# Kernel optimization log

Measured on AMD Instinct MI355X. Metric: run time of the kernel, lower is better.

The kernel has to match this reference:

```python
import jax, jax.numpy as jnp
import numpy as np

N = 100000
E = 1600000
NFEAT, NHID, NCLASS = 500, 128, 40


def setup_inputs() -> dict:
    key = jax.random.key(0)
    ks = jax.random.split(key, 12)
    x = jax.random.normal(ks[0], (N, NFEAT), dtype=jnp.float32)
    row = jax.random.randint(ks[1], (E,), 0, N, dtype=jnp.int32)
    col = jax.random.randint(ks[2], (E,), 0, N, dtype=jnp.int32)
    # precomputed normalized adjacency values (D^-1/2 A D^-1/2 style)
    edge_weight = jax.random.uniform(ks[3], (E,), dtype=jnp.float32) / 16.0
    def lin(k, fi, fo):
        s = 1.0 / np.sqrt(fi)
        return jax.random.uniform(k, (fi, fo), dtype=jnp.float32, minval=-s, maxval=s)
    return {
        "x": x, "row": row, "col": col, "edge_weight": edge_weight,
        "W1": lin(ks[4], NFEAT, NHID), "b1": jnp.zeros((NHID,), jnp.float32),
        "W2": lin(ks[5], NHID, NHID), "b2": jnp.zeros((NHID,), jnp.float32),
        "W3": lin(ks[6], NHID, NHID), "b3": jnp.zeros((NHID,), jnp.float32),
        "W4": lin(ks[7], NHID, NCLASS), "b4": jnp.zeros((NCLASS,), jnp.float32),
    }


def gcn_layer(h, row, col, edge_weight, W, b):
    # support = h @ W ; out = spmm(adj, support) + b  (Kipf GraphConvolution)
    support = h @ W                                   # [N, Fout]
    msgs = edge_weight[:, None] * support[col]        # [E, Fout] gather on source nodes
    agg = jax.ops.segment_sum(msgs, row, num_segments=N)  # scatter-add to dest nodes
    return agg + b


def reference(x, row, col, edge_weight, W1, b1, W2, b2, W3, b3, W4, b4):
    # dropout is identity in eval mode (training=False)
    h = jax.nn.relu(gcn_layer(x, row, col, edge_weight, W1, b1))
    h = jax.nn.relu(gcn_layer(h, row, col, edge_weight, W2, b2))
    h = jax.nn.relu(gcn_layer(h, row, col, edge_weight, W3, b3))
    h = gcn_layer(h, row, col, edge_weight, W4, b4)
    return jax.nn.log_softmax(h, axis=1)
```

## Files before the change

kernel.cpp:

```cpp
#include <hip/hip_runtime.h>
#include <cstdint>
#include <cstddef>

#define NFEAT 500
#define NHID  128
#define NCLASS 40

typedef __attribute__((ext_vector_type(8))) short bf16x8;
typedef __attribute__((ext_vector_type(4))) float f32x4;

__device__ __forceinline__ unsigned short f2bf(float f) {
    union { float f; unsigned u; } v; v.f = f;
    unsigned u = v.u;
    unsigned r = u + 0x7FFF + ((u >> 16) & 1);
    return (unsigned short)(r >> 16);
}
__device__ __forceinline__ float bf2f(unsigned short h) {
    union { unsigned u; float f; } v; v.u = ((unsigned)h) << 16; return v.f;
}


__global__ void k_hist(const int* __restrict__ row, int E, int* __restrict__ counts) {
    int i = blockIdx.x * 256 + threadIdx.x;
    if (i < E) atomicAdd(&counts[row[i]], 1);
}

__global__ void k_block_sum(const int* __restrict__ counts, int n, int* __restrict__ partials) {
    __shared__ int tmp[256];
    int i = blockIdx.x * 256 + threadIdx.x;
    tmp[threadIdx.x] = (i < n) ? counts[i] : 0;
    __syncthreads();
    for (int o = 128; o > 0; o >>= 1) {
        if (threadIdx.x < o) tmp[threadIdx.x] += tmp[threadIdx.x + o];
        __syncthreads();
    }
    if (threadIdx.x == 0) partials[blockIdx.x] = tmp[0];
}

__global__ void k_scan_partials(int* __restrict__ partials, int nb) {
    __shared__ int tmp[512];
    int t = threadIdx.x;
    int v = (t < nb) ? partials[t] : 0;
    tmp[t] = v;
    __syncthreads();
    for (int o = 1; o < 512; o <<= 1) {
        int add = (t >= o) ? tmp[t - o] : 0;
        __syncthreads();
        tmp[t] += add;
        __syncthreads();
    }
    if (t < nb) partials[t] = tmp[t] - v;
}

__global__ void k_scan_counts(int* __restrict__ counts, const int* __restrict__ partials,
                              int* __restrict__ row_ptr, int n) {
    __shared__ int tmp[256];
    int t = threadIdx.x;
    int i = blockIdx.x * 256 + t;
    int v = (i < n) ? counts[i] : 0;
    tmp[t] = v;
    __syncthreads();
    for (int o = 1; o < 256; o <<= 1) {
        int add = (t >= o) ? tmp[t - o] : 0;
        __syncthreads();
        tmp[t] += add;
        __syncthreads();
    }
    int incl = tmp[t];
    int base = partials[blockIdx.x];
    if (i < n) {
        row_ptr[i] = base + incl - v;
        counts[i] = 0;
    }
    if (i == n - 1) row_ptr[n] = base + incl;
}

__global__ void k_scatter(const int* __restrict__ row, const int* __restrict__ col,
                          const float* __restrict__ w, int E,
                          const int* __restrict__ row_ptr, int* __restrict__ cursor,
                          uint2* __restrict__ csr_cw) {
    int i = blockIdx.x * 256 + threadIdx.x;
    if (i < E) {
        int r = row[i];
        int p = row_ptr[r] + atomicAdd(&cursor[r], 1);
        csr_cw[p] = make_uint2((unsigned)col[i], __float_as_uint(w[i]));
    }
}


__global__ void k_prep_w(const float* __restrict__ W, unsigned short* __restrict__ Wt,
                         int K, int Norig, int Nt, int Kpad) {
    int idx = blockIdx.x * 256 + threadIdx.x;
    if (idx >= Nt * Kpad) return;
    int n = idx / Kpad, k = idx % Kpad;
    unsigned short v = 0;
    if (k < K && n < Norig) v = f2bf(W[(size_t)k * Norig + n]);
    Wt[idx] = v;
}


template<bool AFP32, int BN, int CN, int CPITCH>
__global__ __launch_bounds__(256) void k_gemm_mfma(const void* __restrict__ Ain,
                                                   const unsigned short* __restrict__ Wt,
                                                   unsigned short* __restrict__ C,
                                                   int M, int K, int Kpad) {
    constexpr int P = 40;
    constexpr int WGN = (BN == 128) ? 2 : 1;
    constexpr int WGM = 4 / WGN;
    constexpr int TM = 128 / (WGM * 16);
    constexpr int TN = BN / (WGN * 16);
    __shared__ unsigned short As[128][P];
    __shared__ unsigned short Ws[BN][P];

    const int t = threadIdx.x;
    const int lane = t & 63;
    const int w = t >> 6;
    const int wm = w / WGN, wn = w % WGN;
    const int mbase = blockIdx.x * 128;
    const int l15 = lane & 15, quad = lane >> 4;

    const float* Af = (const float*)Ain;
    const unsigned short* Ab = (const unsigned short*)Ain;

    f32x4 acc[TM][TN];
#pragma unroll
    for (int mi = 0; mi < TM; mi++)
#pragma unroll
        for (int ni = 0; ni < TN; ni++)
            acc[mi][ni] = (f32x4){0.f, 0.f, 0.f, 0.f};

    for (int k0 = 0; k0 < Kpad; k0 += 32) {
        if (AFP32) {
#pragma unroll
            for (int p = 0; p < 4; p++) {
                int idx = p * 256 + t;
                int m = idx >> 3, k4 = idx & 7;
                int gm = mbase + m, gk = k0 + k4 * 4;
                float4 v = make_float4(0.f, 0.f, 0.f, 0.f);
                if (gm < M) {
                    if (gk + 3 < K) {
                        v = *(const float4*)(Af + (size_t)gm * K + gk);
                    } else {
                        float tmp[4] = {0.f, 0.f, 0.f, 0.f};
                        for (int j = 0; j < 4; j++)
                            if (gk + j < K) tmp[j] = Af[(size_t)gm * K + gk + j];
                        v = make_float4(tmp[0], tmp[1], tmp[2], tmp[3]);
                    }
                }
                unsigned long long pk = (unsigned long long)f2bf(v.x)
                                      | ((unsigned long long)f2bf(v.y) << 16)
                                      | ((unsigned long long)f2bf(v.z) << 32)
                                      | ((unsigned long long)f2bf(v.w) << 48);
                *(unsigned long long*)&As[m][k4 * 4] = pk;
            }
        } else {
#pragma unroll
            for (int p = 0; p < 2; p++) {
                int idx = p * 256 + t;
                int m = idx >> 2, ch = idx & 3;
                int gm = mbase + m, gk = k0 + ch * 8;
                uint4 v = make_uint4(0u, 0u, 0u, 0u);
                if (gm < M) v = *(const uint4*)(Ab + (size_t)gm * K + gk);
                *(uint4*)&As[m][ch * 8] = v;
            }
        }
        for (int idx = t; idx < BN * 4; idx += 256) {
            int n = idx >> 2, ch = idx & 3;
            uint4 v = *(const uint4*)(Wt + (size_t)n * Kpad + k0 + ch * 8);
            *(uint4*)&Ws[n][ch * 8] = v;
        }
        __syncthreads();

        bf16x8 afr[TM], bfr[TN];
#pragma unroll
        for (int mi = 0; mi < TM; mi++)
            afr[mi] = *(const bf16x8*)&As[wm * (TM * 16) + mi * 16 + l15][quad * 8];
#pragma unroll
        for (int ni = 0; ni < TN; ni++)
            bfr[ni] = *(const bf16x8*)&Ws[wn * (TN * 16) + ni * 16 + l15][quad * 8];
#pragma unroll
        for (int mi = 0; mi < TM; mi++)
#pragma unroll
            for (int ni = 0; ni < TN; ni++)
                acc[mi][ni] = __builtin_amdgcn_mfma_f32_16x16x32_bf16(afr[mi], bfr[ni], acc[mi][ni], 0, 0, 0);
        __syncthreads();
    }

#pragma unroll
    for (int mi = 0; mi < TM; mi++) {
#pragma unroll
        for (int r = 0; r < 4; r++) {
            int gm = mbase + wm * (TM * 16) + mi * 16 + quad * 4 + r;
            if (gm < M) {
#pragma unroll
                for (int ni = 0; ni < TN; ni++) {
                    int gn = wn * (TN * 16) + ni * 16 + l15;
                    if (gn < CN) C[(size_t)gm * CPITCH + gn] = f2bf(acc[mi][ni][r]);
                }
            }
        }
    }
}


__global__ __launch_bounds__(256) void k_spmm128(const unsigned short* __restrict__ S,
                                                 const int* __restrict__ rp,
                                                 const uint2* __restrict__ cw,
                                                 const float* __restrict__ bias,
                                                 unsigned short* __restrict__ out,
                                                 int n, int do_relu) {
    int wid  = threadIdx.x >> 6;
    int lane = threadIdx.x & 63;
    int node = blockIdx.x * 4 + wid;
    if (node >= n) return;
    int s = rp[node], e = rp[node + 1];
    float a0x = 0.f, a0y = 0.f, a1x = 0.f, a1y = 0.f;
    float a2x = 0.f, a2y = 0.f, a3x = 0.f, a3y = 0.f;
    int i = s;
    for (; i + 4 <= e; i += 4) {
        uint2 e0 = cw[i], e1 = cw[i + 1], e2 = cw[i + 2], e3 = cw[i + 3];
        unsigned v0 = ((const unsigned*)(S + (size_t)e0.x * NHID))[lane];
        unsigned v1 = ((const unsigned*)(S + (size_t)e1.x * NHID))[lane];
        unsigned v2 = ((const unsigned*)(S + (size_t)e2.x * NHID))[lane];
        unsigned v3 = ((const unsigned*)(S + (size_t)e3.x * NHID))[lane];
        float w0 = __uint_as_float(e0.y), w1 = __uint_as_float(e1.y);
        float w2 = __uint_as_float(e2.y), w3 = __uint_as_float(e3.y);
        a0x = fmaf(w0, bf2f((unsigned short)v0), a0x); a0y = fmaf(w0, bf2f((unsigned short)(v0 >> 16)), a0y);
        a1x = fmaf(w1, bf2f((unsigned short)v1), a1x); a1y = fmaf(w1, bf2f((unsigned short)(v1 >> 16)), a1y);
        a2x = fmaf(w2, bf2f((unsigned short)v2), a2x); a2y = fmaf(w2, bf2f((unsigned short)(v2 >> 16)), a2y);
        a3x = fmaf(w3, bf2f((unsigned short)v3), a3x); a3y = fmaf(w3, bf2f((unsigned short)(v3 >> 16)), a3y);
    }
    for (; i < e; i++) {
        uint2 e0 = cw[i];
        unsigned v0 = ((const unsigned*)(S + (size_t)e0.x * NHID))[lane];
        float w0 = __uint_as_float(e0.y);
        a0x = fmaf(w0, bf2f((unsigned short)v0), a0x); a0y = fmaf(w0, bf2f((unsigned short)(v0 >> 16)), a0y);
    }
    float ax = (a0x + a1x) + (a2x + a3x) + bias[lane * 2];
    float ay = (a0y + a1y) + (a2y + a3y) + bias[lane * 2 + 1];
    if (do_relu) {
        ax = fmaxf(ax, 0.f);
        ay = fmaxf(ay, 0.f);
    }
    unsigned o = (unsigned)f2bf(ax) | ((unsigned)f2bf(ay) << 16);
    __builtin_nontemporal_store(o, (unsigned*)(out + (size_t)node * NHID) + lane);
}


__global__ __launch_bounds__(256) void k_spmm40_lsm(const unsigned short* __restrict__ S,
                                                    const int* __restrict__ rp,
                                                    const uint2* __restrict__ cw,
                                                    const float* __restrict__ bias,
                                                    float* __restrict__ out,
                                                    int n) {
    int wid  = threadIdx.x >> 6;
    int lane = threadIdx.x & 63;
    int node = blockIdx.x * 4 + wid;
    if (node >= n) return;
    int s = rp[node], e = rp[node + 1];
    float a0 = 0.f, a1 = 0.f, a2 = 0.f, a3 = 0.f;
    int i = s;
    bool act = lane < NCLASS;
    for (; i + 4 <= e; i += 4) {
        uint2 e0 = cw[i], e1 = cw[i + 1], e2 = cw[i + 2], e3 = cw[i + 3];
        if (act) {
            float v0 = bf2f(S[(size_t)e0.x * NCLASS + lane]);
            float v1 = bf2f(S[(size_t)e1.x * NCLASS + lane]);
            float v2 = bf2f(S[(size_t)e2.x * NCLASS + lane]);
            float v3 = bf2f(S[(size_t)e3.x * NCLASS + lane]);
            a0 = fmaf(__uint_as_float(e0.y), v0, a0);
            a1 = fmaf(__uint_as_float(e1.y), v1, a1);
            a2 = fmaf(__uint_as_float(e2.y), v2, a2);
            a3 = fmaf(__uint_as_float(e3.y), v3, a3);
        }
    }
    for (; i < e; i++) {
        uint2 e0 = cw[i];
        if (act) a0 = fmaf(__uint_as_float(e0.y), bf2f(S[(size_t)e0.x * NCLASS + lane]), a0);
    }
    float acc = (a0 + a1) + (a2 + a3);
    float logit = act ? acc + bias[lane] : -INFINITY;
    float m = logit;
#pragma unroll
    for (int o = 32; o >= 1; o >>= 1) m = fmaxf(m, __shfl_xor(m, o, 64));
    float ex = act ? expf(logit - m) : 0.f;
    float ssum = ex;
#pragma unroll
    for (int o = 32; o >= 1; o >>= 1) ssum += __shfl_xor(ssum, o, 64);
    if (act) {
        float r = logit - m - logf(ssum);
        __builtin_nontemporal_store(r, out + (size_t)node * NCLASS + lane);
    }
}


extern "C" void kernel_launch(void* const* d_in, const int* in_sizes, int n_in,
                              void* d_out, int out_size, void* d_ws, size_t ws_size,
                              hipStream_t stream) {
    const float* x  = (const float*)d_in[0];
    const int* row  = (const int*)d_in[1];
    const int* col  = (const int*)d_in[2];
    const float* ew = (const float*)d_in[3];
    const float* W1 = (const float*)d_in[4];
    const float* b1 = (const float*)d_in[5];
    const float* W2 = (const float*)d_in[6];
    const float* b2 = (const float*)d_in[7];
    const float* W3 = (const float*)d_in[8];
    const float* b3 = (const float*)d_in[9];
    const float* W4 = (const float*)d_in[10];
    const float* b4 = (const float*)d_in[11];
    float* out = (float*)d_out;

    const int Nn = in_sizes[0] / NFEAT;
    const int E  = in_sizes[1];
    const int NB = (Nn + 255) / 256;

    char* ws = (char*)d_ws;
    size_t off = 0;
    auto alloc = [&](size_t bytes) {
        size_t o = off;
        off = (off + bytes + 255) & ~(size_t)255;
        return o;
    };
    int*   row_ptr  = (int*)(ws + alloc((size_t)(Nn + 1) * 4));
    int*   counts   = (int*)(ws + alloc((size_t)Nn * 4));
    int*   partials = (int*)(ws + alloc((size_t)NB * 4));
    uint2* csr_cw   = (uint2*)(ws + alloc((size_t)E * 8));
    unsigned short* Sb  = (unsigned short*)(ws + alloc((size_t)Nn * NHID * 2));
    unsigned short* Hb  = (unsigned short*)(ws + alloc((size_t)Nn * NHID * 2));
    unsigned short* S4b = (unsigned short*)(ws + alloc((size_t)Nn * NCLASS * 2 + 256));
    unsigned short* Wt1 = (unsigned short*)(ws + alloc((size_t)128 * 512 * 2));
    unsigned short* Wt2 = (unsigned short*)(ws + alloc((size_t)128 * 128 * 2));
    unsigned short* Wt3 = (unsigned short*)(ws + alloc((size_t)128 * 128 * 2));
    unsigned short* Wt4 = (unsigned short*)(ws + alloc((size_t)48 * 128 * 2));

    k_prep_w<<<(128 * 512 + 255) / 256, 256, 0, stream>>>(W1, Wt1, NFEAT, NHID, 128, 512);
    k_prep_w<<<(128 * 128 + 255) / 256, 256, 0, stream>>>(W2, Wt2, NHID, NHID, 128, 128);
    k_prep_w<<<(128 * 128 + 255) / 256, 256, 0, stream>>>(W3, Wt3, NHID, NHID, 128, 128);
    k_prep_w<<<(48 * 128 + 255) / 256, 256, 0, stream>>>(W4, Wt4, NHID, NCLASS, 48, 128);

    (void)hipMemsetAsync(counts, 0, (size_t)Nn * 4, stream);
    k_hist<<<(E + 255) / 256, 256, 0, stream>>>(row, E, counts);
    k_block_sum<<<NB, 256, 0, stream>>>(counts, Nn, partials);
    k_scan_partials<<<1, 512, 0, stream>>>(partials, NB);
    k_scan_counts<<<NB, 256, 0, stream>>>(counts, partials, row_ptr, Nn);
    k_scatter<<<(E + 255) / 256, 256, 0, stream>>>(row, col, ew, E, row_ptr, counts, csr_cw);

    const int gblocks = (Nn + 127) / 128;
    const int spmm_blocks = (Nn + 3) / 4;

    k_gemm_mfma<true, 128, 128, 128><<<gblocks, 256, 0, stream>>>(x, Wt1, Sb, Nn, NFEAT, 512);
    k_spmm128<<<spmm_blocks, 256, 0, stream>>>(Sb, row_ptr, csr_cw, b1, Hb, Nn, 1);
    k_gemm_mfma<false, 128, 128, 128><<<gblocks, 256, 0, stream>>>(Hb, Wt2, Sb, Nn, NHID, NHID);
    k_spmm128<<<spmm_blocks, 256, 0, stream>>>(Sb, row_ptr, csr_cw, b2, Hb, Nn, 1);
    k_gemm_mfma<false, 128, 128, 128><<<gblocks, 256, 0, stream>>>(Hb, Wt3, Sb, Nn, NHID, NHID);
    k_spmm128<<<spmm_blocks, 256, 0, stream>>>(Sb, row_ptr, csr_cw, b3, Hb, Nn, 1);
    k_gemm_mfma<false, 48, 40, 40><<<gblocks, 256, 0, stream>>>(Hb, Wt4, S4b, Nn, NHID, NHID);
    k_spmm40_lsm<<<spmm_blocks, 256, 0, stream>>>(S4b, row_ptr, csr_cw, b4, out, Nn);
}
```

Baseline: 878.2 us.

## Prefetch next K-tile into registers and halve GEMM M-tile to 64 rows

The MFMA GEMM now loads the next K-slice of A and W into registers while the current slice is computed from LDS, overlapping global loads with MFMA work. The block M-tile shrinks from 128 to 64 rows, doubling the grid for better occupancy across CUs. Intermediate buffers are padded to a multiple of 64 rows so bf16 loads and stores can skip row bounds checks. The costs are extra registers for the staged data and reads of uninitialized padded rows, which are written but never consumed.

```diff
diff --git a/kernel.cpp b/kernel.cpp
--- a/kernel.cpp
+++ b/kernel.cpp
@@ -104,19 +104,20 @@
                                                    const unsigned short* __restrict__ Wt,
                                                    unsigned short* __restrict__ C,
                                                    int M, int K, int Kpad) {
-    constexpr int P = 40;
-    constexpr int WGN = (BN == 128) ? 2 : 1;
-    constexpr int WGM = 4 / WGN;
-    constexpr int TM = 128 / (WGM * 16);
-    constexpr int TN = BN / (WGN * 16);
-    __shared__ unsigned short As[128][P];
+    constexpr int P  = 40;
+    constexpr int NW = (BN == 128) ? 2 : 1;
+    constexpr int MW = 4 / NW;
+    constexpr int TM = 64 / (MW * 16);
+    constexpr int TN = BN / (NW * 16);
+    constexpr int WCH = (BN == 128) ? 2 : 1;
+    __shared__ unsigned short As[64][P];
     __shared__ unsigned short Ws[BN][P];
 
     const int t = threadIdx.x;
     const int lane = t & 63;
     const int w = t >> 6;
-    const int wm = w / WGN, wn = w % WGN;
-    const int mbase = blockIdx.x * 128;
+    const int wm = w / NW, wn = w % NW;
+    const int mbase = blockIdx.x * 64;
     const int l15 = lane & 15, quad = lane >> 4;
 
     const float* Af = (const float*)Ain;
@@ -129,48 +130,73 @@
         for (int ni = 0; ni < TN; ni++)
             acc[mi][ni] = (f32x4){0.f, 0.f, 0.f, 0.f};
 
-    for (int k0 = 0; k0 < Kpad; k0 += 32) {
+    float4 ra_f[2];
+    uint4  ra_b;
+    uint4  rw[WCH];
+
+    auto loadA = [&](int k0) {
         if (AFP32) {
 #pragma unroll
-            for (int p = 0; p < 4; p++) {
+            for (int p = 0; p < 2; p++) {
                 int idx = p * 256 + t;
-                int m = idx >> 3, k4 = idx & 7;
-                int gm = mbase + m, gk = k0 + k4 * 4;
+                int m = idx >> 3, ch = idx & 7;
+                int gm = mbase + m, gk = k0 + ch * 4;
                 float4 v = make_float4(0.f, 0.f, 0.f, 0.f);
-                if (gm < M) {
-                    if (gk + 3 < K) {
-                        v = *(const float4*)(Af + (size_t)gm * K + gk);
-                    } else {
-                        float tmp[4] = {0.f, 0.f, 0.f, 0.f};
-                        for (int j = 0; j < 4; j++)
-                            if (gk + j < K) tmp[j] = Af[(size_t)gm * K + gk + j];
-                        v = make_float4(tmp[0], tmp[1], tmp[2], tmp[3]);
-                    }
-                }
+                if (gm < M && gk < K) v = *(const float4*)(Af + (size_t)gm * K + gk);
+                ra_f[p] = v;
+            }
+        } else {
+            int m = t >> 2, ch = t & 3;
+            ra_b = *(const uint4*)(Ab + (size_t)(mbase + m) * Kpad + k0 + ch * 8);
+        }
+    };
+    auto loadW = [&](int k0) {
+#pragma unroll
+        for (int p = 0; p < WCH; p++) {
+            int idx = p * 256 + t;
+            if (BN * 4 > idx) {
+                int n = idx >> 2, ch = idx & 3;
+                rw[p] = *(const uint4*)(Wt + (size_t)n * Kpad + k0 + ch * 8);
+            }
+        }
+    };
+    auto storeLDS = [&]() {
+        if (AFP32) {
+#pragma unroll
+            for (int p = 0; p < 2; p++) {
+                int idx = p * 256 + t;
+                int m = idx >> 3, ch = idx & 7;
+                float4 v = ra_f[p];
                 unsigned long long pk = (unsigned long long)f2bf(v.x)
                                       | ((unsigned long long)f2bf(v.y) << 16)
                                       | ((unsigned long long)f2bf(v.z) << 32)
                                       | ((unsigned long long)f2bf(v.w) << 48);
-                *(unsigned long long*)&As[m][k4 * 4] = pk;
+                *(unsigned long long*)&As[m][ch * 4] = pk;
             }
         } else {
-#pragma unroll
-            for (int p = 0; p < 2; p++) {
-                int idx = p * 256 + t;
-                int m = idx >> 2, ch = idx & 3;
-                int gm = mbase + m, gk = k0 + ch * 8;
-                uint4 v = make_uint4(0u, 0u, 0u, 0u);
-                if (gm < M) v = *(const uint4*)(Ab + (size_t)gm * K + gk);
-                *(uint4*)&As[m][ch * 8] = v;
-            }
-        }
-        for (int idx = t; idx < BN * 4; idx += 256) {
-            int n = idx >> 2, ch = idx & 3;
-            uint4 v = *(const uint4*)(Wt + (size_t)n * Kpad + k0 + ch * 8);
-            *(uint4*)&Ws[n][ch * 8] = v;
-        }
-        __syncthreads();
-
+            int m = t >> 2, ch = t & 3;
+            *(uint4*)&As[m][ch * 8] = ra_b;
+        }
+#pragma unroll
+        for (int p = 0; p < WCH; p++) {
+            int idx = p * 256 + t;
+            if (BN * 4 > idx) {
+                int n = idx >> 2, ch = idx & 3;
+                *(uint4*)&Ws[n][ch * 8] = rw[p];
+            }
+        }
+    };
+
+    loadA(0);
+    loadW(0);
+    for (int k0 = 0; k0 < Kpad; k0 += 32) {
+        storeLDS();
+        __syncthreads();
+        bool more = (k0 + 32) < Kpad;
+        if (more) {
+            loadA(k0 + 32);
+            loadW(k0 + 32);
+        }
         bf16x8 afr[TM], bfr[TN];
 #pragma unroll
         for (int mi = 0; mi < TM; mi++)
@@ -183,7 +209,7 @@
 #pragma unroll
             for (int ni = 0; ni < TN; ni++)
                 acc[mi][ni] = __builtin_amdgcn_mfma_f32_16x16x32_bf16(afr[mi], bfr[ni], acc[mi][ni], 0, 0, 0);
-        __syncthreads();
+        if (more) __syncthreads();
     }
 
 #pragma unroll
@@ -191,12 +217,10 @@
 #pragma unroll
         for (int r = 0; r < 4; r++) {
             int gm = mbase + wm * (TM * 16) + mi * 16 + quad * 4 + r;
-            if (gm < M) {
-#pragma unroll
-                for (int ni = 0; ni < TN; ni++) {
-                    int gn = wn * (TN * 16) + ni * 16 + l15;
-                    if (gn < CN) C[(size_t)gm * CPITCH + gn] = f2bf(acc[mi][ni][r]);
-                }
+#pragma unroll
+            for (int ni = 0; ni < TN; ni++) {
+                int gn = wn * (TN * 16) + ni * 16 + l15;
+                if (gn < CN) C[(size_t)gm * CPITCH + gn] = f2bf(acc[mi][ni][r]);
             }
         }
     }
@@ -314,6 +338,7 @@
     const int Nn = in_sizes[0] / NFEAT;
     const int E  = in_sizes[1];
     const int NB = (Nn + 255) / 256;
+    const int Mpad = (Nn + 63) & ~63;
 
     char* ws = (char*)d_ws;
     size_t off = 0;
@@ -326,9 +351,9 @@
     int*   counts   = (int*)(ws + alloc((size_t)Nn * 4));
     int*   partials = (int*)(ws + alloc((size_t)NB * 4));
     uint2* csr_cw   = (uint2*)(ws + alloc((size_t)E * 8));
-    unsigned short* Sb  = (unsigned short*)(ws + alloc((size_t)Nn * NHID * 2));
-    unsigned short* Hb  = (unsigned short*)(ws + alloc((size_t)Nn * NHID * 2));
-    unsigned short* S4b = (unsigned short*)(ws + alloc((size_t)Nn * NCLASS * 2 + 256));
+    unsigned short* Sb  = (unsigned short*)(ws + alloc((size_t)Mpad * NHID * 2));
+    unsigned short* Hb  = (unsigned short*)(ws + alloc((size_t)Mpad * NHID * 2));
+    unsigned short* S4b = (unsigned short*)(ws + alloc((size_t)Mpad * NCLASS * 2));
     unsigned short* Wt1 = (unsigned short*)(ws + alloc((size_t)128 * 512 * 2));
     unsigned short* Wt2 = (unsigned short*)(ws + alloc((size_t)128 * 128 * 2));
     unsigned short* Wt3 = (unsigned short*)(ws + alloc((size_t)128 * 128 * 2));
@@ -346,7 +371,7 @@
     k_scan_counts<<<NB, 256, 0, stream>>>(counts, partials, row_ptr, Nn);
     k_scatter<<<(E + 255) / 256, 256, 0, stream>>>(row, col, ew, E, row_ptr, counts, csr_cw);
 
-    const int gblocks = (Nn + 127) / 128;
+    const int gblocks = Mpad / 64;
     const int spmm_blocks = (Nn + 3) / 4;
 
     k_gemm_mfma<true, 128, 128, 128><<<gblocks, 256, 0, stream>>>(x, Wt1, Sb, Nn, NFEAT, 512);
```

Result: slower. 900.8 us (+2.6%).
